# Optimization experiments

Hardware: AMD Instinct MI355X
Metric: run time of the kernel (lower is better)

The kernel has to match this reference:

```python
import jax, jax.numpy as jnp
import numpy as np
from jax import lax

N_NODES = 200000
FEAT = 64
B = 4096
DEG = 32
P = 2048
EMBED = 64
CONTRA = 64
EPS = 1e-8


def _cos(a, b):
    # cosine similarity along last axis, torch-style eps clamp
    num = jnp.sum(a * b, axis=-1)
    na = jnp.sqrt(jnp.sum(a * a, axis=-1))
    nb = jnp.sqrt(jnp.sum(b * b, axis=-1))
    return num / (jnp.maximum(na, EPS) * jnp.maximum(nb, EPS))


def setup_inputs() -> dict:
    key = jax.random.key(0)
    ks = jax.random.split(key, 16)
    return {
        "nodes": jax.random.randint(ks[0], (B,), 0, N_NODES),
        "labels": jax.random.randint(ks[1], (B,), 0, 2),
        "neigh1": jax.random.randint(ks[2], (B, DEG), 0, N_NODES),
        "neigh2": jax.random.randint(ks[3], (B, DEG), 0, N_NODES),
        "neigh3": jax.random.randint(ks[4], (B, DEG), 0, N_NODES),
        "pos_nodes": jax.random.randint(ks[5], (P,), 0, N_NODES),
        "features": jax.random.normal(ks[6], (N_NODES, FEAT), jnp.float32),
        "weight": jax.random.normal(ks[7], (EMBED * 3 + FEAT, EMBED), jnp.float32) * 0.05,
        "rsimTrans": jax.random.normal(ks[8], (FEAT, CONTRA), jnp.float32) * 0.05,
        "pos_embs": jax.random.normal(ks[9], (3, CONTRA), jnp.float32),
        "W1": jax.random.normal(ks[10], (FEAT, EMBED), jnp.float32) * 0.05,
        "W2": jax.random.normal(ks[11], (FEAT, EMBED), jnp.float32) * 0.05,
        "W3": jax.random.normal(ks[12], (FEAT, EMBED), jnp.float32) * 0.05,
        "sample_num": 16,
    }


def _relation(features, rsimTrans, center_orig, center_sim, pos_sim, neigh, pos_emb, W, sample_num):
    n_orig = features[neigh]                               # [B, D, F] irregular gather
    n_sim = jax.nn.relu(jnp.einsum('bdf,fc->bdc', n_orig, rsimTrans))  # [B, D, C]
    neigh_scores = _cos(center_orig[:, None, :], n_orig)   # [B, D]
    neigh_pos_scores = _cos(pos_emb[None, None, :], n_sim) # [B, D]
    pos_scores = _cos(pos_emb[None, :], pos_sim)           # [P]
    center_scores = _cos(pos_emb[None, :], center_sim)     # [B]
    # per-relation sampling: keep top ceil(D*rho) neighbors by pos-similarity
    _, idx = lax.top_k(neigh_pos_scores, sample_num)       # [B, k]
    sampled = jnp.take_along_axis(n_orig, idx[..., None], axis=1)  # [B, k, F]
    agg = jnp.mean(sampled, axis=1)                        # [B, F]
    r_feats = jax.nn.relu(agg @ W)                         # [B, E]
    sampled_pos = jnp.take_along_axis(neigh_pos_scores, idx, axis=1)
    loss = jnp.mean((sampled_pos - jnp.mean(pos_scores)) ** 2)
    return r_feats, loss


def reference(nodes, labels, neigh1, neigh2, neigh3, pos_nodes, features,
              weight, rsimTrans, pos_embs, W1, W2, W3, sample_num):
    center_orig = features[nodes]                              # [B, F]
    center_sim = jax.nn.relu(center_orig @ rsimTrans)          # [B, C]
    pos_sim = jax.nn.relu(features[pos_nodes] @ rsimTrans)     # [P, C]

    r1, l1 = _relation(features, rsimTrans, center_orig, center_sim, pos_sim,
                       neigh1, pos_embs[0], W1, sample_num)
    r2, l2 = _relation(features, rsimTrans, center_orig, center_sim, pos_sim,
                       neigh2, pos_embs[1], W2, sample_num)
    r3, l3 = _relation(features, rsimTrans, center_orig, center_sim, pos_sim,
                       neigh3, pos_embs[2], W3, sample_num)

    cat_feats = jnp.concatenate([center_orig, r1, r2, r3], axis=1)  # [B, F+3E]
    combined = jax.nn.relu(cat_feats @ weight).T                    # [E, B]
    feat_contra_loss = (l1 + l2 + l3) / 3.0
    return combined, feat_contra_loss
```

## Files before the change

kernel.cpp:

```cpp
#include <hip/hip_runtime.h>
#include <hip/hip_bf16.h>

#define NN     200000
#define FEATD  64
#define BN     4096
#define DEG    32
#define PP     2048
#define EMB    64
#define EPSV   1e-8f
#define NTILE64 3125

#define WS_SC    0
#define WS_PL    1000000
#define WS_RF    1100000

typedef short  bf16x8 __attribute__((ext_vector_type(8)));
typedef float  f32x4  __attribute__((ext_vector_type(4)));

__device__ __forceinline__ unsigned int bfr(float x) {
    unsigned int u = __float_as_uint(x);
    return (u + 0x7FFFu + ((u >> 16) & 1u)) & 0xFFFF0000u;
}

__global__ __launch_bounds__(256, 2) void node_precompute(
    const float* __restrict__ features, const float* __restrict__ rsim,
    const float* __restrict__ pos_embs, float4* __restrict__ node_sc)
{
    __shared__ unsigned int lds[4][2][8][64][4];
    __shared__ float4 trp[4][16][16];
    int t = threadIdx.x, w = t >> 6, l = t & 63;
    int tile = blockIdx.x * 4 + w;
    if (tile >= NTILE64) return;
    int lg = l >> 4;
    int lr = l & 15;
    const float4* Gf = (const float4*)features;

    bf16x8 rhi[2][4], rlo[2][4];
#pragma unroll
    for (int kk = 0; kk < 2; ++kk)
#pragma unroll
        for (int nf = 0; nf < 4; ++nf) {
            union { unsigned int u[4]; bf16x8 v; } H, L;
#pragma unroll
            for (int i = 0; i < 4; ++i) {
                int k0 = kk * 32 + lg * 8 + i * 2;
                int j  = nf * 16 + lr;
                float x0 = rsim[k0 * 64 + j];
                float x1 = rsim[(k0 + 1) * 64 + j];
                unsigned int r0 = bfr(x0), r1 = bfr(x1);
                H.u[i] = (r0 >> 16) | r1;
                float l0 = x0 - __uint_as_float(r0);
                float l1 = x1 - __uint_as_float(r1);
                L.u[i] = (__float_as_uint(l0) >> 16)
                       | (__float_as_uint(l1) & 0xFFFF0000u);
            }
            rhi[kk][nf] = H.v; rlo[kk][nf] = L.v;
        }

    float pe[3][4];
#pragma unroll
    for (int rr = 0; rr < 3; ++rr)
#pragma unroll
        for (int nf = 0; nf < 4; ++nf)
            pe[rr][nf] = pos_embs[rr * 64 + nf * 16 + lr];

    unsigned int (*Lhi)[64][4] = lds[w][0];
    unsigned int (*Llo)[64][4] = lds[w][1];
    float4 (*T)[16] = trp[w];

    const float4* src = Gf + (size_t)tile * 1024;
#pragma unroll
    for (int s = 0; s < 16; ++s) {
        float4 v = src[s * 64 + l];
        int node = s * 4 + lg;
        int kg = lr >> 1, half = lr & 1;
        unsigned int rx = bfr(v.x), ry = bfr(v.y);
        unsigned int rz = bfr(v.z), rw = bfr(v.w);
        unsigned int h0 = (rx >> 16) | ry;
        unsigned int h1 = (rz >> 16) | rw;
        float lx = v.x - __uint_as_float(rx), ly = v.y - __uint_as_float(ry);
        float lz = v.z - __uint_as_float(rz), lw = v.w - __uint_as_float(rw);
        unsigned int l0 = (__float_as_uint(lx) >> 16)
                        | (__float_as_uint(ly) & 0xFFFF0000u);
        unsigned int l1 = (__float_as_uint(lz) >> 16)
                        | (__float_as_uint(lw) & 0xFFFF0000u);
        uint2* dh = (uint2*)&Lhi[kg][node ^ kg][half * 2];
        uint2* dl = (uint2*)&Llo[kg][node ^ kg][half * 2];
        *dh = make_uint2(h0, h1);
        *dl = make_uint2(l0, l1);
    }

    const bf16x8* ph = (const bf16x8*)Lhi;
    const bf16x8* pl = (const bf16x8*)Llo;

#pragma unroll
    for (int mf = 0; mf < 4; ++mf) {
        int node = mf * 16 + lr;
        bf16x8 ah0 = ph[lg * 64 + (node ^ lg)];
        bf16x8 ah1 = ph[(4 + lg) * 64 + (node ^ (4 + lg))];
        bf16x8 al0 = pl[lg * 64 + (node ^ lg)];
        bf16x8 al1 = pl[(4 + lg) * 64 + (node ^ (4 + lg))];

        f32x4 acc[4];
#pragma unroll
        for (int nf = 0; nf < 4; ++nf) acc[nf] = (f32x4)(0.f);
#pragma unroll
        for (int nf = 0; nf < 4; ++nf) {
            acc[nf] = __builtin_amdgcn_mfma_f32_16x16x32_bf16(
                          ah0, rhi[0][nf], acc[nf], 0, 0, 0);
            acc[nf] = __builtin_amdgcn_mfma_f32_16x16x32_bf16(
                          ah1, rhi[1][nf], acc[nf], 0, 0, 0);
            acc[nf] = __builtin_amdgcn_mfma_f32_16x16x32_bf16(
                          ah0, rlo[0][nf], acc[nf], 0, 0, 0);
            acc[nf] = __builtin_amdgcn_mfma_f32_16x16x32_bf16(
                          ah1, rlo[1][nf], acc[nf], 0, 0, 0);
            acc[nf] = __builtin_amdgcn_mfma_f32_16x16x32_bf16(
                          al0, rhi[0][nf], acc[nf], 0, 0, 0);
            acc[nf] = __builtin_amdgcn_mfma_f32_16x16x32_bf16(
                          al1, rhi[1][nf], acc[nf], 0, 0, 0);
        }

#pragma unroll
        for (int reg = 0; reg < 4; ++reg) {
            float s0 = 0.f, s1 = 0.f, s2 = 0.f, q = 0.f;
#pragma unroll
            for (int nf = 0; nf < 4; ++nf) {
                float v = fmaxf(acc[nf][reg], 0.f);
                s0 += v * pe[0][nf];
                s1 += v * pe[1][nf];
                s2 += v * pe[2][nf];
                q  += v * v;
            }
            int nd = lg * 4 + reg;
            T[nd][(lr + nd) & 15] = make_float4(s0, s1, s2, q);
        }
        int rn = l >> 2, rq = l & 3;
        float4 a0 = T[rn][(rq * 4 + 0 + rn) & 15];
        float4 a1 = T[rn][(rq * 4 + 1 + rn) & 15];
        float4 a2 = T[rn][(rq * 4 + 2 + rn) & 15];
        float4 a3 = T[rn][(rq * 4 + 3 + rn) & 15];
        float sx = a0.x + a1.x + a2.x + a3.x;
        float sy = a0.y + a1.y + a2.y + a3.y;
        float sz = a0.z + a1.z + a2.z + a3.z;
        float sw = a0.w + a1.w + a2.w + a3.w;
#pragma unroll
        for (int o = 1; o < 4; o <<= 1) {
            sx += __shfl_xor(sx, o);
            sy += __shfl_xor(sy, o);
            sz += __shfl_xor(sz, o);
            sw += __shfl_xor(sw, o);
        }
        if (rq == 0)
            node_sc[tile * 64 + mf * 16 + rn] =
                make_float4(sx, sy, sz, sqrtf(sw));
    }
}

__global__ __launch_bounds__(256) void relation_agg(
    const int* __restrict__ n1, const int* __restrict__ n2, const int* __restrict__ n3,
    const float* __restrict__ features, const float4* __restrict__ node_sc,
    const float* __restrict__ W1, const float* __restrict__ W2, const float* __restrict__ W3,
    const float* __restrict__ pos_embs, float* __restrict__ plossws,
    float* __restrict__ rfeat, const int* __restrict__ smp)
{
    int r = blockIdx.y;
    const int*   neigh = (r == 0) ? n1 : (r == 1) ? n2 : n3;
    const float* W     = (r == 0) ? W1 : (r == 1) ? W2 : W3;
    int k = smp[0];
    int t = threadIdx.x;
    int wv = t >> 6, lane = t & 63;
    int b = blockIdx.x * 4 + wv;

    __shared__ int sel_ids[4][32];
    __shared__ float4 aggl[4][16];

    float pv = pos_embs[r * 64 + lane];
    float qq = pv * pv;
#pragma unroll
    for (int o = 1; o < 64; o <<= 1) qq += __shfl_xor(qq, o);
    float inv_pe = 1.f / fmaxf(sqrtf(qq), EPSV);

    float s = -1e30f;
    int   n = 0;
    if (lane < 32) {
        n = neigh[b * DEG + lane];
        float4 sc = node_sc[n];
        float num = (r == 0) ? sc.x : (r == 1) ? sc.y : sc.z;
        s = num * inv_pe / fmaxf(sc.w, EPSV);
    }
    int cnt = 0;
#pragma unroll
    for (int d2 = 0; d2 < 32; ++d2) {
        float v = __shfl(s, d2);
        cnt += ((v > s) || (v == s && d2 < lane)) ? 1 : 0;
    }
    bool sel = (lane < 32) && (cnt < k);
    if (sel) sel_ids[wv][cnt] = n;

    float sp = sel ? s : 0.f;
    float sq = sel ? s * s : 0.f;
#pragma unroll
    for (int off = 32; off; off >>= 1) {
        sp += __shfl_down(sp, off);
        sq += __shfl_down(sq, off);
    }
    if (lane == 0) {
        int wid = (r * 1024 + blockIdx.x) * 4 + wv;
        plossws[wid * 2]     = sp;
        plossws[wid * 2 + 1] = sq;
    }

    const float4* F = (const float4*)features;
    int col   = lane & 15;
    int rbase = lane >> 4;
    float4 a = make_float4(0.f, 0.f, 0.f, 0.f);
    if (k == 16) {
        int nid0 = sel_ids[wv][rbase];
        int nid1 = sel_ids[wv][rbase + 4];
        int nid2 = sel_ids[wv][rbase + 8];
        int nid3 = sel_ids[wv][rbase + 12];
        float4 v0 = F[(size_t)nid0 * 16 + col];
        float4 v1 = F[(size_t)nid1 * 16 + col];
        float4 v2 = F[(size_t)nid2 * 16 + col];
        float4 v3 = F[(size_t)nid3 * 16 + col];
        a.x = v0.x + v1.x + v2.x + v3.x;
        a.y = v0.y + v1.y + v2.y + v3.y;
        a.z = v0.z + v1.z + v2.z + v3.z;
        a.w = v0.w + v1.w + v2.w + v3.w;
    } else {
        for (int row0 = 0; row0 < k; row0 += 4) {
            int row = row0 + rbase;
            if (row < k) {
                int nid = sel_ids[wv][row];
                float4 v = F[(size_t)nid * 16 + col];
                a.x += v.x; a.y += v.y; a.z += v.z; a.w += v.w;
            }
        }
    }
#pragma unroll
    for (int off = 16; off <= 32; off <<= 1) {
        a.x += __shfl_xor(a.x, off);
        a.y += __shfl_xor(a.y, off);
        a.z += __shfl_xor(a.z, off);
        a.w += __shfl_xor(a.w, off);
    }
    float inv_k = 1.f / (float)k;
    a.x *= inv_k; a.y *= inv_k; a.z *= inv_k; a.w *= inv_k;

    if (lane < 16) aggl[wv][lane] = a;

    float acc = 0.f;
#pragma unroll
    for (int j4 = 0; j4 < 16; ++j4) {
        float4 ag = aggl[wv][j4];
        acc += ag.x * W[(j4 * 4 + 0) * EMB + lane]
             + ag.y * W[(j4 * 4 + 1) * EMB + lane]
             + ag.z * W[(j4 * 4 + 2) * EMB + lane]
             + ag.w * W[(j4 * 4 + 3) * EMB + lane];
    }
    rfeat[((size_t)r * BN + b) * EMB + lane] = fmaxf(acc, 0.f);
}

#define CSTRIDE 264
__global__ __launch_bounds__(256) void final_mm(
    const int* __restrict__ nodes, const float* __restrict__ features,
    const float* __restrict__ rfeat, const float* __restrict__ weight,
    const float* __restrict__ pos_embs, const int* __restrict__ pos_nodes,
    const float4* __restrict__ node_sc, const float* __restrict__ plossws,
    const int* __restrict__ smp, float* __restrict__ out)
{
    __shared__ float cat_b[8 * CSTRIDE];
    __shared__ float trans[8 * 65];
    __shared__ float invpe_sm[3];
    __shared__ float wsum[4][3];
    __shared__ float lsum[4][3][2];
    int t = threadIdx.x;
    int wv = t >> 6, lane = t & 63;
    int b0 = blockIdx.x * 8;

    for (int idx = t; idx < 512; idx += 256) {
        int bb = idx >> 6, f = idx & 63;
        cat_b[bb * CSTRIDE + f] = features[(size_t)nodes[b0 + bb] * FEATD + f];
    }
#pragma unroll
    for (int r = 0; r < 3; ++r)
        for (int idx = t; idx < 512; idx += 256) {
            int bb = idx >> 6, j = idx & 63;
            cat_b[bb * CSTRIDE + 64 + r * 64 + j] =
                rfeat[((size_t)r * BN + b0 + bb) * EMB + j];
        }
    __syncthreads();

    int bb0 = wv * 2;
    float acc0 = 0.f, acc1 = 0.f;
    const float* c0p = &cat_b[bb0 * CSTRIDE];
    const float* c1p = &cat_b[(bb0 + 1) * CSTRIDE];
    for (int i0 = 0; i0 < 256; i0 += 16) {
        float w[16];
#pragma unroll
        for (int u = 0; u < 16; ++u)
            w[u] = weight[(i0 + u) * EMB + lane];
#pragma unroll
        for (int u = 0; u < 16; ++u) {
            acc0 += w[u] * c0p[i0 + u];
            acc1 += w[u] * c1p[i0 + u];
        }
    }
    trans[bb0 * 65 + lane]       = fmaxf(acc0, 0.f);
    trans[(bb0 + 1) * 65 + lane] = fmaxf(acc1, 0.f);
    __syncthreads();

    for (int idx = t; idx < 512; idx += 256) {
        int e = idx >> 3, bb = idx & 7;
        out[(size_t)e * BN + b0 + bb] = trans[bb * 65 + e];
    }

    if (blockIdx.x != 0) return;

    float pv = (t < 192) ? pos_embs[t] : 0.f;
    float q = pv * pv;
#pragma unroll
    for (int o = 1; o < 64; o <<= 1) q += __shfl_xor(q, o);
    if (t < 192 && lane == 0)
        invpe_sm[wv] = 1.f / fmaxf(sqrtf(q), EPSV);
    __syncthreads();

    float m0 = 0.f, m1 = 0.f, m2 = 0.f;
    for (int p = t; p < PP; p += 256) {
        int n = pos_nodes[p];
        float4 sc = node_sc[n];
        float invn = 1.f / fmaxf(sc.w, EPSV);
        m0 += sc.x * invpe_sm[0] * invn;
        m1 += sc.y * invpe_sm[1] * invn;
        m2 += sc.z * invpe_sm[2] * invn;
    }
#pragma unroll
    for (int o = 1; o < 64; o <<= 1) {
        m0 += __shfl_xor(m0, o);
        m1 += __shfl_xor(m1, o);
        m2 += __shfl_xor(m2, o);
    }
    if (lane == 0) { wsum[wv][0] = m0; wsum[wv][1] = m1; wsum[wv][2] = m2; }

    if (wv < 3) {
        float s1 = 0.f, s2 = 0.f;
        const float2* pl2 = (const float2*)plossws;
        for (int i = lane; i < 4096; i += 64) {
            float2 v = pl2[wv * 4096 + i];
            s1 += v.x; s2 += v.y;
        }
#pragma unroll
        for (int o = 1; o < 64; o <<= 1) {
            s1 += __shfl_xor(s1, o);
            s2 += __shfl_xor(s2, o);
        }
        if (lane == 0) { lsum[0][wv][0] = s1; lsum[0][wv][1] = s2; }
    }
    __syncthreads();

    if (t == 0) {
        int k = smp[0];
        float N = (float)BN * (float)k;
        float loss = 0.f;
#pragma unroll
        for (int r = 0; r < 3; ++r) {
            float mp = (wsum[0][r] + wsum[1][r] + wsum[2][r] + wsum[3][r])
                       / (float)PP;
            float s1 = lsum[0][r][0], s2 = lsum[0][r][1];
            loss += s2 / N - 2.f * mp * s1 / N + mp * mp;
        }
        out[(size_t)EMB * BN] = loss / 3.f;
    }
}

extern "C" void kernel_launch(void* const* d_in, const int* in_sizes, int n_in,
                              void* d_out, int out_size, void* d_ws, size_t ws_size,
                              hipStream_t stream) {
    const int*   nodes     = (const int*)  d_in[0];
    const int*   neigh1    = (const int*)  d_in[2];
    const int*   neigh2    = (const int*)  d_in[3];
    const int*   neigh3    = (const int*)  d_in[4];
    const int*   pos_nodes = (const int*)  d_in[5];
    const float* features  = (const float*)d_in[6];
    const float* weight    = (const float*)d_in[7];
    const float* rsim      = (const float*)d_in[8];
    const float* pos_embs  = (const float*)d_in[9];
    const float* W1        = (const float*)d_in[10];
    const float* W2        = (const float*)d_in[11];
    const float* W3        = (const float*)d_in[12];
    const int*   smp       = (const int*)  d_in[13];
    float* out = (float*)d_out;
    float* ws  = (float*)d_ws;

    float4* node_sc = (float4*)(ws + WS_SC);
    float*  plossws = ws + WS_PL;
    float*  rfeat   = ws + WS_RF;

    node_precompute<<<dim3((NTILE64 + 3) / 4), dim3(256), 0, stream>>>(
        features, rsim, pos_embs, node_sc);
    relation_agg<<<dim3(BN / 4, 3), dim3(256), 0, stream>>>(
        neigh1, neigh2, neigh3, features, node_sc, W1, W2, W3,
        pos_embs, plossws, rfeat, smp);
    final_mm<<<dim3(BN / 8), dim3(256), 0, stream>>>(
        nodes, features, rfeat, weight, pos_embs, pos_nodes,
        node_sc, plossws, smp, out);
}
```

Measured before the change: 70.14 us.

## Halve node_precompute tile size and replace LDS transpose with shuffle reduction

Each wave now handles 32 nodes instead of 64, which halves LDS per block and raises the launch-bounds occupancy hint from 2 to 4 blocks per CU, giving more waves to hide global-load latency. The per-node reduction across the 16 column lanes now uses xor shuffles over four accumulators instead of an LDS transpose buffer. pos_embs is staged once in shared memory rather than held in registers. The shuffle reduction issues more cross-lane operations, and the shared pos_embs reads add LDS traffic inside the inner loop.

```diff
diff --git a/kernel.cpp b/kernel.cpp
--- a/kernel.cpp
+++ b/kernel.cpp
@@ -8,7 +8,7 @@
 #define PP     2048
 #define EMB    64
 #define EPSV   1e-8f
-#define NTILE64 3125
+#define NTILE32 6250
 
 #define WS_SC    0
 #define WS_PL    1000000
@@ -22,18 +22,18 @@
     return (u + 0x7FFFu + ((u >> 16) & 1u)) & 0xFFFF0000u;
 }
 
-__global__ __launch_bounds__(256, 2) void node_precompute(
+__global__ __launch_bounds__(256, 4) void node_precompute(
     const float* __restrict__ features, const float* __restrict__ rsim,
     const float* __restrict__ pos_embs, float4* __restrict__ node_sc)
 {
-    __shared__ unsigned int lds[4][2][8][64][4];
-    __shared__ float4 trp[4][16][16];
+    __shared__ unsigned int lds[4][2][8][32][4];
+    __shared__ float pel[192];
     int t = threadIdx.x, w = t >> 6, l = t & 63;
-    int tile = blockIdx.x * 4 + w;
-    if (tile >= NTILE64) return;
     int lg = l >> 4;
     int lr = l & 15;
     const float4* Gf = (const float4*)features;
+
+    if (t < 192) pel[t] = pos_embs[t];
 
     bf16x8 rhi[2][4], rlo[2][4];
 #pragma unroll
@@ -57,20 +57,15 @@
             rhi[kk][nf] = H.v; rlo[kk][nf] = L.v;
         }
 
-    float pe[3][4];
-#pragma unroll
-    for (int rr = 0; rr < 3; ++rr)
-#pragma unroll
-        for (int nf = 0; nf < 4; ++nf)
-            pe[rr][nf] = pos_embs[rr * 64 + nf * 16 + lr];
-
-    unsigned int (*Lhi)[64][4] = lds[w][0];
-    unsigned int (*Llo)[64][4] = lds[w][1];
-    float4 (*T)[16] = trp[w];
-
-    const float4* src = Gf + (size_t)tile * 1024;
-#pragma unroll
-    for (int s = 0; s < 16; ++s) {
+    int tile = blockIdx.x * 4 + w;
+    if (tile >= NTILE32) return;
+
+    unsigned int (*Lhi)[32][4] = lds[w][0];
+    unsigned int (*Llo)[32][4] = lds[w][1];
+
+    const float4* src = Gf + (size_t)tile * 512;
+#pragma unroll
+    for (int s = 0; s < 8; ++s) {
         float4 v = src[s * 64 + l];
         int node = s * 4 + lg;
         int kg = lr >> 1, half = lr & 1;
@@ -94,12 +89,12 @@
     const bf16x8* pl = (const bf16x8*)Llo;
 
 #pragma unroll
-    for (int mf = 0; mf < 4; ++mf) {
+    for (int mf = 0; mf < 2; ++mf) {
         int node = mf * 16 + lr;
-        bf16x8 ah0 = ph[lg * 64 + (node ^ lg)];
-        bf16x8 ah1 = ph[(4 + lg) * 64 + (node ^ (4 + lg))];
-        bf16x8 al0 = pl[lg * 64 + (node ^ lg)];
-        bf16x8 al1 = pl[(4 + lg) * 64 + (node ^ (4 + lg))];
+        bf16x8 ah0 = ph[lg * 32 + (node ^ lg)];
+        bf16x8 ah1 = ph[(4 + lg) * 32 + (node ^ (4 + lg))];
+        bf16x8 al0 = pl[lg * 32 + (node ^ lg)];
+        bf16x8 al1 = pl[(4 + lg) * 32 + (node ^ (4 + lg))];
 
         f32x4 acc[4];
 #pragma unroll
@@ -120,39 +115,37 @@
                           al1, rhi[1][nf], acc[nf], 0, 0, 0);
         }
 
-#pragma unroll
-        for (int reg = 0; reg < 4; ++reg) {
-            float s0 = 0.f, s1 = 0.f, s2 = 0.f, q = 0.f;
+        float q[4] = {0,0,0,0}, s0[4] = {0,0,0,0};
+        float s1[4] = {0,0,0,0}, s2[4] = {0,0,0,0};
+#pragma unroll
+        for (int reg = 0; reg < 4; ++reg)
 #pragma unroll
             for (int nf = 0; nf < 4; ++nf) {
                 float v = fmaxf(acc[nf][reg], 0.f);
-                s0 += v * pe[0][nf];
-                s1 += v * pe[1][nf];
-                s2 += v * pe[2][nf];
-                q  += v * v;
+                int j = nf * 16 + lr;
+                q[reg]  += v * v;
+                s0[reg] += v * pel[j];
+                s1[reg] += v * pel[64 + j];
+                s2[reg] += v * pel[128 + j];
             }
-            int nd = lg * 4 + reg;
-            T[nd][(lr + nd) & 15] = make_float4(s0, s1, s2, q);
-        }
-        int rn = l >> 2, rq = l & 3;
-        float4 a0 = T[rn][(rq * 4 + 0 + rn) & 15];
-        float4 a1 = T[rn][(rq * 4 + 1 + rn) & 15];
-        float4 a2 = T[rn][(rq * 4 + 2 + rn) & 15];
-        float4 a3 = T[rn][(rq * 4 + 3 + rn) & 15];
-        float sx = a0.x + a1.x + a2.x + a3.x;
-        float sy = a0.y + a1.y + a2.y + a3.y;
-        float sz = a0.z + a1.z + a2.z + a3.z;
-        float sw = a0.w + a1.w + a2.w + a3.w;
-#pragma unroll
-        for (int o = 1; o < 4; o <<= 1) {
-            sx += __shfl_xor(sx, o);
-            sy += __shfl_xor(sy, o);
-            sz += __shfl_xor(sz, o);
-            sw += __shfl_xor(sw, o);
-        }
-        if (rq == 0)
-            node_sc[tile * 64 + mf * 16 + rn] =
-                make_float4(sx, sy, sz, sqrtf(sw));
+#pragma unroll
+        for (int o = 1; o < 16; o <<= 1)
+#pragma unroll
+            for (int reg = 0; reg < 4; ++reg) {
+                q[reg]  += __shfl_xor(q[reg],  o);
+                s0[reg] += __shfl_xor(s0[reg], o);
+                s1[reg] += __shfl_xor(s1[reg], o);
+                s2[reg] += __shfl_xor(s2[reg], o);
+            }
+        if (lr < 4) {
+            int r = l & 3;
+            float o0 = (r==0)?s0[0]:(r==1)?s0[1]:(r==2)?s0[2]:s0[3];
+            float o1 = (r==0)?s1[0]:(r==1)?s1[1]:(r==2)?s1[2]:s1[3];
+            float o2 = (r==0)?s2[0]:(r==1)?s2[1]:(r==2)?s2[2]:s2[3];
+            float oq = (r==0)?q[0] :(r==1)?q[1] :(r==2)?q[2] :q[3];
+            node_sc[tile * 32 + mf * 16 + lg * 4 + r] =
+                make_float4(o0, o1, o2, sqrtf(oq));
+        }
     }
 }
 
@@ -273,7 +266,7 @@
     __shared__ float trans[8 * 65];
     __shared__ float invpe_sm[3];
     __shared__ float wsum[4][3];
-    __shared__ float lsum[4][3][2];
+    __shared__ float lsum[3][2];
     int t = threadIdx.x;
     int wv = t >> 6, lane = t & 63;
     int b0 = blockIdx.x * 8;
@@ -354,7 +347,7 @@
             s1 += __shfl_xor(s1, o);
             s2 += __shfl_xor(s2, o);
         }
-        if (lane == 0) { lsum[0][wv][0] = s1; lsum[0][wv][1] = s2; }
+        if (lane == 0) { lsum[wv][0] = s1; lsum[wv][1] = s2; }
     }
     __syncthreads();
 
@@ -366,7 +359,7 @@
         for (int r = 0; r < 3; ++r) {
             float mp = (wsum[0][r] + wsum[1][r] + wsum[2][r] + wsum[3][r])
                        / (float)PP;
-            float s1 = lsum[0][r][0], s2 = lsum[0][r][1];
+            float s1 = lsum[r][0], s2 = lsum[r][1];
             loss += s2 / N - 2.f * mp * s1 / N + mp * mp;
         }
         out[(size_t)EMB * BN] = loss / 3.f;
@@ -396,7 +389,7 @@
     float*  plossws = ws + WS_PL;
     float*  rfeat   = ws + WS_RF;
 
-    node_precompute<<<dim3((NTILE64 + 3) / 4), dim3(256), 0, stream>>>(
+    node_precompute<<<dim3((NTILE32 + 3) / 4), dim3(256), 0, stream>>>(
         features, rsim, pos_embs, node_sc);
     relation_agg<<<dim3(BN / 4, 3), dim3(256), 0, stream>>>(
         neigh1, neigh2, neigh3, features, node_sc, W1, W2, W3,
```

Result: no change. 70.35 us (+0.3%).
